# Performance work log

Hardware: AMD Instinct MI355X
Metric: run time of the kernel (lower is better)

## Reference

```python
import jax, jax.numpy as jnp
import numpy as np

B, D, H, W, C = 4, 8, 16, 16, 512
K_RED = 8
R = C // K_RED          # reduced channels for Q/K
EPS = 1e-3              # keras LayerNormalization default epsilon


def setup_inputs() -> dict:
    key = jax.random.key(0)
    ks = jax.random.split(key, 8)
    s = 0.02
    f32 = jnp.float32
    return {
        "x":  jax.random.normal(ks[0], (B, D, H, W, C), f32),
        # 1x1x1 Conv3D == per-position linear over channels
        "wq": (jax.random.normal(ks[1], (C, R), f32) * s), "bq": jnp.zeros((R,), f32),
        "wk": (jax.random.normal(ks[2], (C, R), f32) * s), "bk": jnp.zeros((R,), f32),
        "wv": (jax.random.normal(ks[3], (C, C), f32) * s), "bv": jnp.zeros((C,), f32),
        "wm": (jax.random.normal(ks[4], (C, C), f32) * s), "bm": jnp.zeros((C,), f32),
        "g1": jnp.ones((C,), f32), "b1": jnp.zeros((C,), f32),
        "g2": jnp.ones((C,), f32), "b2": jnp.zeros((C,), f32),
    }


def _layer_norm(x, g, b):
    m = jnp.mean(x, axis=-1, keepdims=True)
    v = jnp.mean(jnp.square(x - m), axis=-1, keepdims=True)
    return (x - m) * jax.lax.rsqrt(v + EPS) * g + b


def reference(x, wq, bq, wk, bk, wv, bv, wm, bm, g1, b1, g2, b2):
    b, d, h, w, c = x.shape
    f = h * w
    xf = x.reshape(b, d, f, c)                      # [B,D,F,C]
    Q = xf @ wq + bq                                # [B,D,F,R]
    K = xf @ wk + bk                                # [B,D,F,R]
    V = xf @ wv + bv                                # [B,D,F,C]
    # full global scores: [B, D, F, D, F]
    e = jnp.einsum('bifr,bgjr->bifgj', Q, K)
    alphas = jax.nn.softmax(e.reshape(b, d, f, d * f), axis=-1)
    alphas = alphas.reshape(b, d, f, d, f)
    # original einsum 'bdfgh,bdhi->bdfi' sums over key-depth g and uses V at
    # the query depth d; fold the g-sum first, then per-depth F x F matmul.
    a2 = alphas.sum(axis=3)                         # [B,D,F,F]
    attn = jnp.einsum('bdfh,bdhc->bdfc', a2, V)     # [B,D,F,C]
    y1 = _layer_norm(attn + xf, g1, b1)
    y2 = _layer_norm(y1 + jax.nn.relu(y1 @ wm + bm), g2, b2)
    return y2.reshape(b, d, h, w, c)
```

## Files before the change

kernel.cpp:

```cpp
#include <hip/hip_runtime.h>
#include <cstdint>

#define LN_EPS 1e-3f
using u16 = unsigned short;
using u32 = unsigned int;
typedef __attribute__((ext_vector_type(8))) short bh8;
typedef __attribute__((ext_vector_type(4))) float f4;
#define MFMA16(A,B,C) __builtin_amdgcn_mfma_f32_16x16x32_bf16((A),(B),(C),0,0,0)
#define LKBAR() do{ asm volatile("s_waitcnt lgkmcnt(0)" ::: "memory"); \
                    __builtin_amdgcn_s_barrier(); asm volatile("" ::: "memory"); }while(0)

__device__ __forceinline__ u16 bf16r(float f){
    union{float f;u32 u;} c; c.f=f;
    return (u16)((c.u + 0x7fffu + ((c.u>>16)&1u))>>16);
}
__device__ __forceinline__ u32 pk2(float a, float b){
    return (u32)bf16r(a) | ((u32)bf16r(b)<<16);
}

__global__ __launch_bounds__(256) void k0_prep(
    const float* __restrict__ wq, const float* __restrict__ wk,
    const float* __restrict__ wv, const float* __restrict__ wm,
    u16* __restrict__ wqkv_p, u16* __restrict__ wm_p)
{
    const int t = threadIdx.x;
    const int c = t & 15, qn = t >> 4;
    const int quad = qn & 3, ntl = qn >> 2;
    const int blk = blockIdx.x;
    if (blk < 32){
        const int s = blk >> 1, hh = blk & 1;
        const int krow = s*32 + quad*8;
        u16* dst = wqkv_p + (size_t)s*20480;
        #pragma unroll
        for (int i=0;i<5;++i){
            const int nt = hh*20 + i*4 + ntl;
            const int n = nt*16 + c;
            const float* src; int ldw;
            if (n < 64){ src = wq + (size_t)krow*64 + n; ldw = 64; }
            else if (n < 128){ src = wk + (size_t)krow*64 + (n-64); ldw = 64; }
            else { src = wv + (size_t)krow*512 + (n-128); ldw = 512; }
            float v[8];
            #pragma unroll
            for (int j=0;j<8;++j) v[j] = src[(size_t)j*ldw];
            uint4 o; o.x=pk2(v[0],v[1]); o.y=pk2(v[2],v[3]); o.z=pk2(v[4],v[5]); o.w=pk2(v[6],v[7]);
            *(uint4*)&dst[((nt*4+quad)*16 + c)*8] = o;
        }
    } else {
        const int bb = blk - 32;
        const int s = bb >> 1, hh = bb & 1;
        const int krow = s*32 + quad*8;
        u16* dst = wm_p + (size_t)s*16384;
        #pragma unroll
        for (int i=0;i<4;++i){
            const int nt = hh*16 + i*4 + ntl;
            const int n = nt*16 + c;
            const float* src = wm + (size_t)krow*512 + n;
            float v[8];
            #pragma unroll
            for (int j=0;j<8;++j) v[j] = src[(size_t)j*512];
            uint4 o; o.x=pk2(v[0],v[1]); o.y=pk2(v[2],v[3]); o.z=pk2(v[4],v[5]); o.w=pk2(v[6],v[7]);
            *(uint4*)&dst[((nt*4+quad)*16 + c)*8] = o;
        }
    }
}

__global__ __launch_bounds__(512) void k1_qkv(
    const float* __restrict__ x, const float* __restrict__ bq, const float* __restrict__ bk,
    const u16* __restrict__ wqkv_p,
    u16* __restrict__ Qb, u16* __restrict__ Kb, u16* __restrict__ Vb)
{
    __shared__ u16 Asf[16384];
    const int t = threadIdx.x, w = t>>6, lane = t&63, quad = (lane>>4)&3, c = lane&15;
    const int rowbase = blockIdx.x << 5;

    bh8 bw[5];
    #pragma unroll
    for (int nt2=0;nt2<5;++nt2)
        bw[nt2] = *(const bh8*)&wqkv_p[(size_t)((w*5+nt2)*4 + quad)*128 + c*8];
    #pragma unroll
    for (int i=0;i<8;++i){
        const int idx = t + (i<<9);
        const int fr = idx >> 7, fc4 = idx & 127;
        float4 xv = *(const float4*)&x[(size_t)(rowbase+fr)*512 + fc4*4];
        uint2 pkv; pkv.x = pk2(xv.x,xv.y); pkv.y = pk2(xv.z,xv.w);
        const int s = fc4 >> 3, qd = (fc4 >> 1) & 3, j0 = (fc4 & 1)*4;
        *(uint2*)&Asf[(fr>>4)*8192 + s*512 + (qd*16 + (fr&15))*8 + j0] = pkv;
    }
    f4 acc[2][5];
    #pragma unroll
    for (int rt=0;rt<2;++rt)
        #pragma unroll
        for (int i=0;i<5;++i) acc[rt][i] = (f4){0.f,0.f,0.f,0.f};
    __syncthreads();

    #pragma unroll
    for (int s=0;s<16;++s){
        bh8 bn[5];
        if (s+1 < 16){
            #pragma unroll
            for (int nt2=0;nt2<5;++nt2)
                bn[nt2] = *(const bh8*)&wqkv_p[(size_t)(s+1)*20480 + ((w*5+nt2)*4 + quad)*128 + c*8];
        }
        bh8 a[2];
        #pragma unroll
        for (int rt=0;rt<2;++rt)
            a[rt] = *(const bh8*)&Asf[rt*8192 + s*512 + (quad*16+c)*8];
        __builtin_amdgcn_s_setprio(1);
        #pragma unroll
        for (int rt=0;rt<2;++rt)
            #pragma unroll
            for (int nt2=0;nt2<5;++nt2)
                acc[rt][nt2] = MFMA16(a[rt], bw[nt2], acc[rt][nt2]);
        __builtin_amdgcn_s_setprio(0);
        if (s+1 < 16){
            #pragma unroll
            for (int nt2=0;nt2<5;++nt2) bw[nt2] = bn[nt2];
        }
    }

    const int bd = rowbase >> 8;
    #pragma unroll
    for (int rt=0;rt<2;++rt){
        const int rtg = (blockIdx.x<<1) + rt;
        const int kloc = (rowbase & 255) + rt*16 + quad*4;
        const int sv = kloc >> 5, kq = (kloc >> 3) & 3, jk0 = kloc & 7;
        #pragma unroll
        for (int nt2=0;nt2<5;++nt2){
            const int colb = w*80 + nt2*16;
            if (colb < 128){
                const bool isK = (colb >= 64);
                const int r = colb - (isK ? 64 : 0) + c;
                const float bias = isK ? bk[r] : bq[r];
                u16* dstb = (isK ? Kb : Qb) + ((size_t)(rtg*2 + (r>>5))*4 + ((r>>3)&3))*128 + (r&7);
                #pragma unroll
                for (int reg=0;reg<4;++reg)
                    dstb[(quad*4+reg)*8] = bf16r(acc[rt][nt2][reg] + bias);
            } else {
                const int ntv = (colb - 128) >> 4;
                u16* dstv = Vb + (size_t)bd*131072 + (size_t)sv*16384
                               + (size_t)((ntv*4+kq)*128 + c*8 + jk0);
                ushort4 o;
                o.x = bf16r(acc[rt][nt2][0]); o.y = bf16r(acc[rt][nt2][1]);
                o.z = bf16r(acc[rt][nt2][2]); o.w = bf16r(acc[rt][nt2][3]);
                *(ushort4*)dstv = o;
            }
        }
    }
}

__global__ __launch_bounds__(512) void k234(
    const u16* __restrict__ Qb, const u16* __restrict__ Kb, const u16* __restrict__ Vb,
    const u16* __restrict__ wm_p,
    const float* __restrict__ x, const float* __restrict__ bv,
    const float* __restrict__ g1, const float* __restrict__ b1,
    const float* __restrict__ bm, const float* __restrict__ g2, const float* __restrict__ b2,
    float* __restrict__ out)
{
    __shared__ u16 U[16384];
    __shared__ float redA[256], redB[256];
    const int t = threadIdx.x, w = t>>6, lane = t&63, quad = (lane>>4)&3, c = lane&15;
    const int bd = blockIdx.x & 31, ftile = blockIdx.x >> 5;
    const int b = bd >> 3;
    const int rowbase = (bd<<8) + (ftile<<5);
    const int rt00 = rowbase >> 4;
    const u16* Kp = Kb + (size_t)b*131072;
    const u16* Vp = Vb + (size_t)bd*131072;

    bh8 aq[2][2];
    #pragma unroll
    for (int rt=0;rt<2;++rt)
        #pragma unroll
        for (int kk=0;kk<2;++kk)
            aq[rt][kk] = *(const bh8*)&Qb[(size_t)(rt00+rt)*1024 + kk*512 + (quad*16+c)*8];

    float a2r[2][2][4] = {};
    bh8 bk0[2][2];
    #pragma unroll
    for (int kt=0;kt<2;++kt)
        #pragma unroll
        for (int kk=0;kk<2;++kk)
            bk0[kt][kk] = *(const bh8*)&Kp[(size_t)(w*2+kt)*1024 + kk*512 + (quad*16+c)*8];
    #pragma unroll
    for (int cc=0; cc<8; ++cc){
        bh8 bn[2][2];
        if (cc+1 < 8){
            #pragma unroll
            for (int kt=0;kt<2;++kt)
                #pragma unroll
                for (int kk=0;kk<2;++kk)
                    bn[kt][kk] = *(const bh8*)&Kp[(size_t)((cc+1)*16 + w*2+kt)*1024 + kk*512 + (quad*16+c)*8];
        }
        f4 sa[2][2];
        __builtin_amdgcn_s_setprio(1);
        #pragma unroll
        for (int rt=0;rt<2;++rt)
            #pragma unroll
            for (int kt=0;kt<2;++kt){
                sa[rt][kt] = (f4){0.f,0.f,0.f,0.f};
                sa[rt][kt] = MFMA16(aq[rt][0], bk0[kt][0], sa[rt][kt]);
                sa[rt][kt] = MFMA16(aq[rt][1], bk0[kt][1], sa[rt][kt]);
            }
        __builtin_amdgcn_s_setprio(0);
        #pragma unroll
        for (int rt=0;rt<2;++rt)
            #pragma unroll
            for (int kt=0;kt<2;++kt)
                #pragma unroll
                for (int reg=0;reg<4;++reg)
                    a2r[rt][kt][reg] += __expf(sa[rt][kt][reg]);
        if (cc+1 < 8){
            #pragma unroll
            for (int kt=0;kt<2;++kt)
                #pragma unroll
                for (int kk=0;kk<2;++kk) bk0[kt][kk] = bn[kt][kk];
        }
    }
    bh8 bv8[4];
    #pragma unroll
    for (int nt2=0;nt2<4;++nt2)
        bv8[nt2] = *(const bh8*)&Vp[(size_t)((w*4+nt2)*4 + quad)*128 + c*8];
    float lp[2][4];
    #pragma unroll
    for (int rt=0;rt<2;++rt)
        #pragma unroll
        for (int reg=0;reg<4;++reg){
            float v = a2r[rt][0][reg] + a2r[rt][1][reg];
            v += __shfl_xor(v,1,64); v += __shfl_xor(v,2,64);
            v += __shfl_xor(v,4,64); v += __shfl_xor(v,8,64);
            lp[rt][reg] = v;
        }
    if (c==0){
        #pragma unroll
        for (int rt=0;rt<2;++rt)
            #pragma unroll
            for (int reg=0;reg<4;++reg) redA[w*32 + rt*16 + quad*4+reg] = lp[rt][reg];
    }
    LKBAR();
    float fac[2][4];
    #pragma unroll
    for (int rt=0;rt<2;++rt)
        #pragma unroll
        for (int reg=0;reg<4;++reg){
            const int q = rt*16 + quad*4 + reg;
            float s = 0.f;
            #pragma unroll
            for (int ww=0;ww<8;++ww) s += redA[ww*32 + q];
            fac[rt][reg] = 1.f/s;
        }
    #pragma unroll
    for (int rt=0;rt<2;++rt)
        #pragma unroll
        for (int kt=0;kt<2;++kt)
            #pragma unroll
            for (int reg=0;reg<4;++reg){
                const int jp = w*32 + kt*16 + c;
                U[rt*4096 + (jp>>5)*512 + (((jp>>3)&3)*16 + quad*4+reg)*8 + (jp&7)]
                    = bf16r(a2r[rt][kt][reg]*fac[rt][reg]);
            }
    LKBAR();

    float xr[2][4][4];
    #pragma unroll
    for (int rt=0;rt<2;++rt)
        #pragma unroll
        for (int nt2=0;nt2<4;++nt2){
            const int col = w*64 + nt2*16 + c;
            #pragma unroll
            for (int reg=0;reg<4;++reg){
                const int row = rowbase + rt*16 + quad*4 + reg;
                xr[rt][nt2][reg] = x[(size_t)row*512 + col];
            }
        }

    f4 cacc[2][4];
    #pragma unroll
    for (int rt=0;rt<2;++rt)
        #pragma unroll
        for (int i=0;i<4;++i) cacc[rt][i] = (f4){0.f,0.f,0.f,0.f};
    #pragma unroll
    for (int s8=0;s8<8;++s8){
        bh8 bn[4];
        if (s8+1 < 8){
            #pragma unroll
            for (int nt2=0;nt2<4;++nt2)
                bn[nt2] = *(const bh8*)&Vp[(size_t)(s8+1)*16384 + ((w*4+nt2)*4 + quad)*128 + c*8];
        }
        bh8 a[2];
        #pragma unroll
        for (int rt=0;rt<2;++rt)
            a[rt] = *(const bh8*)&U[rt*4096 + s8*512 + (quad*16+c)*8];
        __builtin_amdgcn_s_setprio(1);
        #pragma unroll
        for (int rt=0;rt<2;++rt)
            #pragma unroll
            for (int nt2=0;nt2<4;++nt2)
                cacc[rt][nt2] = MFMA16(a[rt], bv8[nt2], cacc[rt][nt2]);
        __builtin_amdgcn_s_setprio(0);
        if (s8+1 < 8){
            #pragma unroll
            for (int nt2=0;nt2<4;++nt2) bv8[nt2] = bn[nt2];
        }
    }
    bh8 bm8[4];
    #pragma unroll
    for (int nt2=0;nt2<4;++nt2)
        bm8[nt2] = *(const bh8*)&wm_p[(size_t)((w*4+nt2)*4 + quad)*128 + c*8];

    float mean1[2][4], rstd1[2][4];
    {
        float sv4[2][4] = {}, qv2[2][4] = {};
        #pragma unroll
        for (int rt=0;rt<2;++rt)
            #pragma unroll
            for (int nt2=0;nt2<4;++nt2){
                const int col = w*64 + nt2*16 + c;
                const float bvv = bv[col];
                #pragma unroll
                for (int reg=0;reg<4;++reg){
                    float val = cacc[rt][nt2][reg] + bvv + xr[rt][nt2][reg];
                    cacc[rt][nt2][reg] = val;
                    sv4[rt][reg] += val; qv2[rt][reg] = fmaf(val,val,qv2[rt][reg]);
                }
            }
        #pragma unroll
        for (int rt=0;rt<2;++rt)
            #pragma unroll
            for (int reg=0;reg<4;++reg){
                float s1=sv4[rt][reg], s2=qv2[rt][reg];
                s1 += __shfl_xor(s1,1,64); s2 += __shfl_xor(s2,1,64);
                s1 += __shfl_xor(s1,2,64); s2 += __shfl_xor(s2,2,64);
                s1 += __shfl_xor(s1,4,64); s2 += __shfl_xor(s2,4,64);
                s1 += __shfl_xor(s1,8,64); s2 += __shfl_xor(s2,8,64);
                sv4[rt][reg]=s1; qv2[rt][reg]=s2;
            }
        if (c==0){
            #pragma unroll
            for (int rt=0;rt<2;++rt)
                #pragma unroll
                for (int reg=0;reg<4;++reg){
                    redA[w*32 + rt*16 + quad*4+reg]=sv4[rt][reg];
                    redB[w*32 + rt*16 + quad*4+reg]=qv2[rt][reg];
                }
        }
        LKBAR();
        #pragma unroll
        for (int rt=0;rt<2;++rt)
            #pragma unroll
            for (int reg=0;reg<4;++reg){
                const int q = rt*16 + quad*4 + reg;
                float S=0.f, Q2=0.f;
                #pragma unroll
                for (int ww=0;ww<8;++ww){ S += redA[ww*32+q]; Q2 += redB[ww*32+q]; }
                const float m = S*(1.f/512.f);
                mean1[rt][reg]=m; rstd1[rt][reg]=rsqrtf(Q2*(1.f/512.f) - m*m + LN_EPS);
            }
        #pragma unroll
        for (int rt=0;rt<2;++rt)
            #pragma unroll
            for (int nt2=0;nt2<4;++nt2){
                const int col = w*64 + nt2*16 + c;
                const float gg = g1[col], bb1 = b1[col];
                #pragma unroll
                for (int reg=0;reg<4;++reg){
                    float y = (cacc[rt][nt2][reg]-mean1[rt][reg])*rstd1[rt][reg]*gg + bb1;
                    cacc[rt][nt2][reg] = y;
                    U[rt*8192 + (col>>5)*512 + (((col>>3)&3)*16 + quad*4+reg)*8 + (col&7)] = bf16r(y);
                }
            }
        LKBAR();
    }

    f4 dacc[2][4];
    #pragma unroll
    for (int rt=0;rt<2;++rt)
        #pragma unroll
        for (int i=0;i<4;++i) dacc[rt][i] = (f4){0.f,0.f,0.f,0.f};
    #pragma unroll
    for (int s=0;s<16;++s){
        bh8 bn[4];
        if (s+1 < 16){
            #pragma unroll
            for (int nt2=0;nt2<4;++nt2)
                bn[nt2] = *(const bh8*)&wm_p[(size_t)(s+1)*16384 + ((w*4+nt2)*4 + quad)*128 + c*8];
        }
        bh8 a[2];
        #pragma unroll
        for (int rt=0;rt<2;++rt)
            a[rt] = *(const bh8*)&U[rt*8192 + s*512 + (quad*16+c)*8];
        __builtin_amdgcn_s_setprio(1);
        #pragma unroll
        for (int rt=0;rt<2;++rt)
            #pragma unroll
            for (int nt2=0;nt2<4;++nt2)
                dacc[rt][nt2] = MFMA16(a[rt], bm8[nt2], dacc[rt][nt2]);
        __builtin_amdgcn_s_setprio(0);
        if (s+1 < 16){
            #pragma unroll
            for (int nt2=0;nt2<4;++nt2) bm8[nt2] = bn[nt2];
        }
    }

    {
        float sv4[2][4] = {}, qv2[2][4] = {};
        #pragma unroll
        for (int rt=0;rt<2;++rt)
            #pragma unroll
            for (int nt2=0;nt2<4;++nt2){
                const int col = w*64 + nt2*16 + c;
                const float bmv = bm[col];
                #pragma unroll
                for (int reg=0;reg<4;++reg){
                    float hh = fmaxf(dacc[rt][nt2][reg]+bmv, 0.f) + cacc[rt][nt2][reg];
                    dacc[rt][nt2][reg] = hh;
                    sv4[rt][reg] += hh; qv2[rt][reg] = fmaf(hh,hh,qv2[rt][reg]);
                }
            }
        #pragma unroll
        for (int rt=0;rt<2;++rt)
            #pragma unroll
            for (int reg=0;reg<4;++reg){
                float s1=sv4[rt][reg], s2=qv2[rt][reg];
                s1 += __shfl_xor(s1,1,64); s2 += __shfl_xor(s2,1,64);
                s1 += __shfl_xor(s1,2,64); s2 += __shfl_xor(s2,2,64);
                s1 += __shfl_xor(s1,4,64); s2 += __shfl_xor(s2,4,64);
                s1 += __shfl_xor(s1,8,64); s2 += __shfl_xor(s2,8,64);
                sv4[rt][reg]=s1; qv2[rt][reg]=s2;
            }
        if (c==0){
            #pragma unroll
            for (int rt=0;rt<2;++rt)
                #pragma unroll
                for (int reg=0;reg<4;++reg){
                    redA[w*32 + rt*16 + quad*4+reg]=sv4[rt][reg];
                    redB[w*32 + rt*16 + quad*4+reg]=qv2[rt][reg];
                }
        }
        LKBAR();
        #pragma unroll
        for (int rt=0;rt<2;++rt){
            float mean[4], rstd[4];
            #pragma unroll
            for (int reg=0;reg<4;++reg){
                const int q = rt*16 + quad*4 + reg;
                float S=0.f, Q2=0.f;
                #pragma unroll
                for (int ww=0;ww<8;++ww){ S += redA[ww*32+q]; Q2 += redB[ww*32+q]; }
                const float m = S*(1.f/512.f);
                mean[reg]=m; rstd[reg]=rsqrtf(Q2*(1.f/512.f) - m*m + LN_EPS);
            }
            #pragma unroll
            for (int nt2=0;nt2<4;++nt2){
                const int col = w*64 + nt2*16 + c;
                const float gg = g2[col], bb2 = b2[col];
                #pragma unroll
                for (int reg=0;reg<4;++reg){
                    const int row = rowbase + rt*16 + quad*4 + reg;
                    out[(size_t)row*512 + col] = (dacc[rt][nt2][reg]-mean[reg])*rstd[reg]*gg + bb2;
                }
            }
        }
    }
}

extern "C" void kernel_launch(void* const* d_in, const int* in_sizes, int n_in,
                              void* d_out, int out_size, void* d_ws, size_t ws_size,
                              hipStream_t stream) {
    (void)in_sizes; (void)n_in; (void)out_size; (void)ws_size;
    const float* x  = (const float*)d_in[0];
    const float* wq = (const float*)d_in[1];
    const float* bq = (const float*)d_in[2];
    const float* wk = (const float*)d_in[3];
    const float* bk = (const float*)d_in[4];
    const float* wv = (const float*)d_in[5];
    const float* bv = (const float*)d_in[6];
    const float* wm = (const float*)d_in[7];
    const float* bm = (const float*)d_in[8];
    const float* g1 = (const float*)d_in[9];
    const float* b1 = (const float*)d_in[10];
    const float* g2 = (const float*)d_in[11];
    const float* b2 = (const float*)d_in[12];

    u16* wqkv_p = (u16*)d_ws;
    u16* wm_p   = wqkv_p + 327680;
    u16* Qb     = wm_p   + 262144;
    u16* Kb     = Qb     + 524288;
    u16* Vb     = Kb     + 524288;
    float* outp = (float*)d_out;

    k0_prep<<<64, 256, 0, stream>>>(wq, wk, wv, wm, wqkv_p, wm_p);
    k1_qkv <<<256, 512, 0, stream>>>(x, bq, bk, wqkv_p, Qb, Kb, Vb);
    k234   <<<256, 512, 0, stream>>>(Qb, Kb, Vb, wm_p, x, bv, g1, b1, bm, g2, b2, outp);
}
```

Before: 124.6 us.

## Fuse three kernels into one cooperative kernel with grid syncs

Merges the weight-prep, QKV projection and attention/LN/MLP kernels into a single cooperative launch of 256 blocks, separated by threadfence plus grid.sync barriers. The aim is to remove two kernel launch gaps and the inter-kernel drain/ramp. In exchange every block pays two grid-wide barriers. The fused kernel also needs both shared buffers at once, which raises LDS and register use per block and may cut occupancy.

```diff
diff --git a/kernel.cpp b/kernel.cpp
--- a/kernel.cpp
+++ b/kernel.cpp
@@ -1,6 +1,8 @@
 #include <hip/hip_runtime.h>
+#include <hip/hip_cooperative_groups.h>
 #include <cstdint>
 
+namespace cg = cooperative_groups;
 #define LN_EPS 1e-3f
 using u16 = unsigned short;
 using u32 = unsigned int;
@@ -18,444 +20,445 @@
     return (u32)bf16r(a) | ((u32)bf16r(b)<<16);
 }
 
-__global__ __launch_bounds__(256) void k0_prep(
-    const float* __restrict__ wq, const float* __restrict__ wk,
-    const float* __restrict__ wv, const float* __restrict__ wm,
-    u16* __restrict__ wqkv_p, u16* __restrict__ wm_p)
-{
-    const int t = threadIdx.x;
-    const int c = t & 15, qn = t >> 4;
-    const int quad = qn & 3, ntl = qn >> 2;
-    const int blk = blockIdx.x;
-    if (blk < 32){
-        const int s = blk >> 1, hh = blk & 1;
-        const int krow = s*32 + quad*8;
-        u16* dst = wqkv_p + (size_t)s*20480;
-        #pragma unroll
-        for (int i=0;i<5;++i){
-            const int nt = hh*20 + i*4 + ntl;
-            const int n = nt*16 + c;
-            const float* src; int ldw;
-            if (n < 64){ src = wq + (size_t)krow*64 + n; ldw = 64; }
-            else if (n < 128){ src = wk + (size_t)krow*64 + (n-64); ldw = 64; }
-            else { src = wv + (size_t)krow*512 + (n-128); ldw = 512; }
-            float v[8];
-            #pragma unroll
-            for (int j=0;j<8;++j) v[j] = src[(size_t)j*ldw];
-            uint4 o; o.x=pk2(v[0],v[1]); o.y=pk2(v[2],v[3]); o.z=pk2(v[4],v[5]); o.w=pk2(v[6],v[7]);
-            *(uint4*)&dst[((nt*4+quad)*16 + c)*8] = o;
-        }
-    } else {
-        const int bb = blk - 32;
-        const int s = bb >> 1, hh = bb & 1;
-        const int krow = s*32 + quad*8;
-        u16* dst = wm_p + (size_t)s*16384;
-        #pragma unroll
-        for (int i=0;i<4;++i){
-            const int nt = hh*16 + i*4 + ntl;
-            const int n = nt*16 + c;
-            const float* src = wm + (size_t)krow*512 + n;
-            float v[8];
-            #pragma unroll
-            for (int j=0;j<8;++j) v[j] = src[(size_t)j*512];
-            uint4 o; o.x=pk2(v[0],v[1]); o.y=pk2(v[2],v[3]); o.z=pk2(v[4],v[5]); o.w=pk2(v[6],v[7]);
-            *(uint4*)&dst[((nt*4+quad)*16 + c)*8] = o;
-        }
-    }
-}
-
-__global__ __launch_bounds__(512) void k1_qkv(
-    const float* __restrict__ x, const float* __restrict__ bq, const float* __restrict__ bk,
-    const u16* __restrict__ wqkv_p,
-    u16* __restrict__ Qb, u16* __restrict__ Kb, u16* __restrict__ Vb)
+__global__ __launch_bounds__(512) void fused_all(
+    const float* __restrict__ x,
+    const float* __restrict__ wq, const float* __restrict__ bq,
+    const float* __restrict__ wk, const float* __restrict__ bk,
+    const float* __restrict__ wv, const float* __restrict__ bv,
+    const float* __restrict__ wm, const float* __restrict__ bm,
+    const float* __restrict__ g1, const float* __restrict__ b1,
+    const float* __restrict__ g2, const float* __restrict__ b2,
+    u16* __restrict__ wqkv_p, u16* __restrict__ wm_p,
+    u16* __restrict__ Qb, u16* __restrict__ Kb, u16* __restrict__ Vb,
+    float* __restrict__ out)
 {
     __shared__ u16 Asf[16384];
-    const int t = threadIdx.x, w = t>>6, lane = t&63, quad = (lane>>4)&3, c = lane&15;
-    const int rowbase = blockIdx.x << 5;
-
-    bh8 bw[5];
-    #pragma unroll
-    for (int nt2=0;nt2<5;++nt2)
-        bw[nt2] = *(const bh8*)&wqkv_p[(size_t)((w*5+nt2)*4 + quad)*128 + c*8];
-    #pragma unroll
-    for (int i=0;i<8;++i){
-        const int idx = t + (i<<9);
-        const int fr = idx >> 7, fc4 = idx & 127;
-        float4 xv = *(const float4*)&x[(size_t)(rowbase+fr)*512 + fc4*4];
-        uint2 pkv; pkv.x = pk2(xv.x,xv.y); pkv.y = pk2(xv.z,xv.w);
-        const int s = fc4 >> 3, qd = (fc4 >> 1) & 3, j0 = (fc4 & 1)*4;
-        *(uint2*)&Asf[(fr>>4)*8192 + s*512 + (qd*16 + (fr&15))*8 + j0] = pkv;
-    }
-    f4 acc[2][5];
-    #pragma unroll
-    for (int rt=0;rt<2;++rt)
-        #pragma unroll
-        for (int i=0;i<5;++i) acc[rt][i] = (f4){0.f,0.f,0.f,0.f};
-    __syncthreads();
-
-    #pragma unroll
-    for (int s=0;s<16;++s){
-        bh8 bn[5];
-        if (s+1 < 16){
-            #pragma unroll
-            for (int nt2=0;nt2<5;++nt2)
-                bn[nt2] = *(const bh8*)&wqkv_p[(size_t)(s+1)*20480 + ((w*5+nt2)*4 + quad)*128 + c*8];
-        }
-        bh8 a[2];
-        #pragma unroll
-        for (int rt=0;rt<2;++rt)
-            a[rt] = *(const bh8*)&Asf[rt*8192 + s*512 + (quad*16+c)*8];
-        __builtin_amdgcn_s_setprio(1);
-        #pragma unroll
-        for (int rt=0;rt<2;++rt)
-            #pragma unroll
-            for (int nt2=0;nt2<5;++nt2)
-                acc[rt][nt2] = MFMA16(a[rt], bw[nt2], acc[rt][nt2]);
-        __builtin_amdgcn_s_setprio(0);
-        if (s+1 < 16){
-            #pragma unroll
-            for (int nt2=0;nt2<5;++nt2) bw[nt2] = bn[nt2];
-        }
-    }
-
-    const int bd = rowbase >> 8;
-    #pragma unroll
-    for (int rt=0;rt<2;++rt){
-        const int rtg = (blockIdx.x<<1) + rt;
-        const int kloc = (rowbase & 255) + rt*16 + quad*4;
-        const int sv = kloc >> 5, kq = (kloc >> 3) & 3, jk0 = kloc & 7;
-        #pragma unroll
-        for (int nt2=0;nt2<5;++nt2){
-            const int colb = w*80 + nt2*16;
-            if (colb < 128){
-                const bool isK = (colb >= 64);
-                const int r = colb - (isK ? 64 : 0) + c;
-                const float bias = isK ? bk[r] : bq[r];
-                u16* dstb = (isK ? Kb : Qb) + ((size_t)(rtg*2 + (r>>5))*4 + ((r>>3)&3))*128 + (r&7);
-                #pragma unroll
-                for (int reg=0;reg<4;++reg)
-                    dstb[(quad*4+reg)*8] = bf16r(acc[rt][nt2][reg] + bias);
-            } else {
-                const int ntv = (colb - 128) >> 4;
-                u16* dstv = Vb + (size_t)bd*131072 + (size_t)sv*16384
-                               + (size_t)((ntv*4+kq)*128 + c*8 + jk0);
-                ushort4 o;
-                o.x = bf16r(acc[rt][nt2][0]); o.y = bf16r(acc[rt][nt2][1]);
-                o.z = bf16r(acc[rt][nt2][2]); o.w = bf16r(acc[rt][nt2][3]);
-                *(ushort4*)dstv = o;
-            }
-        }
-    }
-}
-
-__global__ __launch_bounds__(512) void k234(
-    const u16* __restrict__ Qb, const u16* __restrict__ Kb, const u16* __restrict__ Vb,
-    const u16* __restrict__ wm_p,
-    const float* __restrict__ x, const float* __restrict__ bv,
-    const float* __restrict__ g1, const float* __restrict__ b1,
-    const float* __restrict__ bm, const float* __restrict__ g2, const float* __restrict__ b2,
-    float* __restrict__ out)
-{
     __shared__ u16 U[16384];
     __shared__ float redA[256], redB[256];
+    cg::grid_group grid = cg::this_grid();
     const int t = threadIdx.x, w = t>>6, lane = t&63, quad = (lane>>4)&3, c = lane&15;
-    const int bd = blockIdx.x & 31, ftile = blockIdx.x >> 5;
-    const int b = bd >> 3;
-    const int rowbase = (bd<<8) + (ftile<<5);
-    const int rt00 = rowbase >> 4;
-    const u16* Kp = Kb + (size_t)b*131072;
-    const u16* Vp = Vb + (size_t)bd*131072;
-
-    bh8 aq[2][2];
-    #pragma unroll
-    for (int rt=0;rt<2;++rt)
-        #pragma unroll
-        for (int kk=0;kk<2;++kk)
-            aq[rt][kk] = *(const bh8*)&Qb[(size_t)(rt00+rt)*1024 + kk*512 + (quad*16+c)*8];
-
-    float a2r[2][2][4] = {};
-    bh8 bk0[2][2];
-    #pragma unroll
-    for (int kt=0;kt<2;++kt)
-        #pragma unroll
-        for (int kk=0;kk<2;++kk)
-            bk0[kt][kk] = *(const bh8*)&Kp[(size_t)(w*2+kt)*1024 + kk*512 + (quad*16+c)*8];
-    #pragma unroll
-    for (int cc=0; cc<8; ++cc){
-        bh8 bn[2][2];
-        if (cc+1 < 8){
+
+    if (blockIdx.x < 64 && t < 256){
+        const int c0 = t & 15, qn = t >> 4;
+        const int q0 = qn & 3, ntl = qn >> 2;
+        const int blk = blockIdx.x;
+        if (blk < 32){
+            const int s = blk >> 1, hh = blk & 1;
+            const int krow = s*32 + q0*8;
+            u16* dst = wqkv_p + (size_t)s*20480;
+            #pragma unroll
+            for (int i=0;i<5;++i){
+                const int nt = hh*20 + i*4 + ntl;
+                const int n = nt*16 + c0;
+                const float* src; int ldw;
+                if (n < 64){ src = wq + (size_t)krow*64 + n; ldw = 64; }
+                else if (n < 128){ src = wk + (size_t)krow*64 + (n-64); ldw = 64; }
+                else { src = wv + (size_t)krow*512 + (n-128); ldw = 512; }
+                float v[8];
+                #pragma unroll
+                for (int j=0;j<8;++j) v[j] = src[(size_t)j*ldw];
+                uint4 o; o.x=pk2(v[0],v[1]); o.y=pk2(v[2],v[3]); o.z=pk2(v[4],v[5]); o.w=pk2(v[6],v[7]);
+                *(uint4*)&dst[((nt*4+q0)*16 + c0)*8] = o;
+            }
+        } else {
+            const int bb = blk - 32;
+            const int s = bb >> 1, hh = bb & 1;
+            const int krow = s*32 + q0*8;
+            u16* dst = wm_p + (size_t)s*16384;
+            #pragma unroll
+            for (int i=0;i<4;++i){
+                const int nt = hh*16 + i*4 + ntl;
+                const int n = nt*16 + c0;
+                const float* src = wm + (size_t)krow*512 + n;
+                float v[8];
+                #pragma unroll
+                for (int j=0;j<8;++j) v[j] = src[(size_t)j*512];
+                uint4 o; o.x=pk2(v[0],v[1]); o.y=pk2(v[2],v[3]); o.z=pk2(v[4],v[5]); o.w=pk2(v[6],v[7]);
+                *(uint4*)&dst[((nt*4+q0)*16 + c0)*8] = o;
+            }
+        }
+    }
+    __threadfence();
+    grid.sync();
+
+    {
+        const int rowbase = blockIdx.x << 5;
+        bh8 bw[5];
+        #pragma unroll
+        for (int nt2=0;nt2<5;++nt2)
+            bw[nt2] = *(const bh8*)&wqkv_p[(size_t)((w*5+nt2)*4 + quad)*128 + c*8];
+        #pragma unroll
+        for (int i=0;i<8;++i){
+            const int idx = t + (i<<9);
+            const int fr = idx >> 7, fc4 = idx & 127;
+            float4 xv = *(const float4*)&x[(size_t)(rowbase+fr)*512 + fc4*4];
+            uint2 pkv; pkv.x = pk2(xv.x,xv.y); pkv.y = pk2(xv.z,xv.w);
+            const int s = fc4 >> 3, qd = (fc4 >> 1) & 3, j0 = (fc4 & 1)*4;
+            *(uint2*)&Asf[(fr>>4)*8192 + s*512 + (qd*16 + (fr&15))*8 + j0] = pkv;
+        }
+        f4 acc[2][5];
+        #pragma unroll
+        for (int rt=0;rt<2;++rt)
+            #pragma unroll
+            for (int i=0;i<5;++i) acc[rt][i] = (f4){0.f,0.f,0.f,0.f};
+        __syncthreads();
+
+        #pragma unroll
+        for (int s=0;s<16;++s){
+            bh8 bn[5];
+            if (s+1 < 16){
+                #pragma unroll
+                for (int nt2=0;nt2<5;++nt2)
+                    bn[nt2] = *(const bh8*)&wqkv_p[(size_t)(s+1)*20480 + ((w*5+nt2)*4 + quad)*128 + c*8];
+            }
+            bh8 a[2];
+            #pragma unroll
+            for (int rt=0;rt<2;++rt)
+                a[rt] = *(const bh8*)&Asf[rt*8192 + s*512 + (quad*16+c)*8];
+            __builtin_amdgcn_s_setprio(1);
+            #pragma unroll
+            for (int rt=0;rt<2;++rt)
+                #pragma unroll
+                for (int nt2=0;nt2<5;++nt2)
+                    acc[rt][nt2] = MFMA16(a[rt], bw[nt2], acc[rt][nt2]);
+            __builtin_amdgcn_s_setprio(0);
+            if (s+1 < 16){
+                #pragma unroll
+                for (int nt2=0;nt2<5;++nt2) bw[nt2] = bn[nt2];
+            }
+        }
+
+        const int bd = rowbase >> 8;
+        #pragma unroll
+        for (int rt=0;rt<2;++rt){
+            const int rtg = (blockIdx.x<<1) + rt;
+            const int kloc = (rowbase & 255) + rt*16 + quad*4;
+            const int sv = kloc >> 5, kq = (kloc >> 3) & 3, jk0 = kloc & 7;
+            #pragma unroll
+            for (int nt2=0;nt2<5;++nt2){
+                const int colb = w*80 + nt2*16;
+                if (colb < 128){
+                    const bool isK = (colb >= 64);
+                    const int r = colb - (isK ? 64 : 0) + c;
+                    const float bias = isK ? bk[r] : bq[r];
+                    u16* dstb = (isK ? Kb : Qb) + ((size_t)(rtg*2 + (r>>5))*4 + ((r>>3)&3))*128 + (r&7);
+                    #pragma unroll
+                    for (int reg=0;reg<4;++reg)
+                        dstb[(quad*4+reg)*8] = bf16r(acc[rt][nt2][reg] + bias);
+                } else {
+                    const int ntv = (colb - 128) >> 4;
+                    u16* dstv = Vb + (size_t)bd*131072 + (size_t)sv*16384
+                                   + (size_t)((ntv*4+kq)*128 + c*8 + jk0);
+                    ushort4 o;
+                    o.x = bf16r(acc[rt][nt2][0]); o.y = bf16r(acc[rt][nt2][1]);
+                    o.z = bf16r(acc[rt][nt2][2]); o.w = bf16r(acc[rt][nt2][3]);
+                    *(ushort4*)dstv = o;
+                }
+            }
+        }
+    }
+    __threadfence();
+    grid.sync();
+
+    {
+        const int bd = blockIdx.x & 31, ftile = blockIdx.x >> 5;
+        const int b = bd >> 3;
+        const int rowbase = (bd<<8) + (ftile<<5);
+        const int rt00 = rowbase >> 4;
+        const u16* Kp = Kb + (size_t)b*131072;
+        const u16* Vp = Vb + (size_t)bd*131072;
+
+        bh8 aq[2][2];
+        #pragma unroll
+        for (int rt=0;rt<2;++rt)
+            #pragma unroll
+            for (int kk=0;kk<2;++kk)
+                aq[rt][kk] = *(const bh8*)&Qb[(size_t)(rt00+rt)*1024 + kk*512 + (quad*16+c)*8];
+
+        float a2r[2][2][4] = {};
+        bh8 bk0[2][2];
+        #pragma unroll
+        for (int kt=0;kt<2;++kt)
+            #pragma unroll
+            for (int kk=0;kk<2;++kk)
+                bk0[kt][kk] = *(const bh8*)&Kp[(size_t)(w*2+kt)*1024 + kk*512 + (quad*16+c)*8];
+        #pragma unroll
+        for (int cc=0; cc<8; ++cc){
+            bh8 bn[2][2];
+            if (cc+1 < 8){
+                #pragma unroll
+                for (int kt=0;kt<2;++kt)
+                    #pragma unroll
+                    for (int kk=0;kk<2;++kk)
+                        bn[kt][kk] = *(const bh8*)&Kp[(size_t)((cc+1)*16 + w*2+kt)*1024 + kk*512 + (quad*16+c)*8];
+            }
+            f4 sa[2][2];
+            __builtin_amdgcn_s_setprio(1);
+            #pragma unroll
+            for (int rt=0;rt<2;++rt)
+                #pragma unroll
+                for (int kt=0;kt<2;++kt){
+                    sa[rt][kt] = (f4){0.f,0.f,0.f,0.f};
+                    sa[rt][kt] = MFMA16(aq[rt][0], bk0[kt][0], sa[rt][kt]);
+                    sa[rt][kt] = MFMA16(aq[rt][1], bk0[kt][1], sa[rt][kt]);
+                }
+            __builtin_amdgcn_s_setprio(0);
+            #pragma unroll
+            for (int rt=0;rt<2;++rt)
+                #pragma unroll
+                for (int kt=0;kt<2;++kt)
+                    #pragma unroll
+                    for (int reg=0;reg<4;++reg)
+                        a2r[rt][kt][reg] += __expf(sa[rt][kt][reg]);
+            if (cc+1 < 8){
+                #pragma unroll
+                for (int kt=0;kt<2;++kt)
+                    #pragma unroll
+                    for (int kk=0;kk<2;++kk) bk0[kt][kk] = bn[kt][kk];
+            }
+        }
+        bh8 bv8[4];
+        #pragma unroll
+        for (int nt2=0;nt2<4;++nt2)
+            bv8[nt2] = *(const bh8*)&Vp[(size_t)((w*4+nt2)*4 + quad)*128 + c*8];
+        float lp[2][4];
+        #pragma unroll
+        for (int rt=0;rt<2;++rt)
+            #pragma unroll
+            for (int reg=0;reg<4;++reg){
+                float v = a2r[rt][0][reg] + a2r[rt][1][reg];
+                v += __shfl_xor(v,1,64); v += __shfl_xor(v,2,64);
+                v += __shfl_xor(v,4,64); v += __shfl_xor(v,8,64);
+                lp[rt][reg] = v;
+            }
+        if (c==0){
+            #pragma unroll
+            for (int rt=0;rt<2;++rt)
+                #pragma unroll
+                for (int reg=0;reg<4;++reg) redA[w*32 + rt*16 + quad*4+reg] = lp[rt][reg];
+        }
+        LKBAR();
+        float fac[2][4];
+        #pragma unroll
+        for (int rt=0;rt<2;++rt)
+            #pragma unroll
+            for (int reg=0;reg<4;++reg){
+                const int q = rt*16 + quad*4 + reg;
+                float s = 0.f;
+                #pragma unroll
+                for (int ww=0;ww<8;++ww) s += redA[ww*32 + q];
+                fac[rt][reg] = 1.f/s;
+            }
+        #pragma unroll
+        for (int rt=0;rt<2;++rt)
             #pragma unroll
             for (int kt=0;kt<2;++kt)
                 #pragma unroll
-                for (int kk=0;kk<2;++kk)
-                    bn[kt][kk] = *(const bh8*)&Kp[(size_t)((cc+1)*16 + w*2+kt)*1024 + kk*512 + (quad*16+c)*8];
-        }
-        f4 sa[2][2];
-        __builtin_amdgcn_s_setprio(1);
-        #pragma unroll
-        for (int rt=0;rt<2;++rt)
-            #pragma unroll
-            for (int kt=0;kt<2;++kt){
-                sa[rt][kt] = (f4){0.f,0.f,0.f,0.f};
-                sa[rt][kt] = MFMA16(aq[rt][0], bk0[kt][0], sa[rt][kt]);
-                sa[rt][kt] = MFMA16(aq[rt][1], bk0[kt][1], sa[rt][kt]);
-            }
-        __builtin_amdgcn_s_setprio(0);
-        #pragma unroll
-        for (int rt=0;rt<2;++rt)
-            #pragma unroll
-            for (int kt=0;kt<2;++kt)
-                #pragma unroll
-                for (int reg=0;reg<4;++reg)
-                    a2r[rt][kt][reg] += __expf(sa[rt][kt][reg]);
-        if (cc+1 < 8){
-            #pragma unroll
-            for (int kt=0;kt<2;++kt)
-                #pragma unroll
-                for (int kk=0;kk<2;++kk) bk0[kt][kk] = bn[kt][kk];
-        }
-    }
-    bh8 bv8[4];
-    #pragma unroll
-    for (int nt2=0;nt2<4;++nt2)
-        bv8[nt2] = *(const bh8*)&Vp[(size_t)((w*4+nt2)*4 + quad)*128 + c*8];
-    float lp[2][4];
-    #pragma unroll
-    for (int rt=0;rt<2;++rt)
-        #pragma unroll
-        for (int reg=0;reg<4;++reg){
-            float v = a2r[rt][0][reg] + a2r[rt][1][reg];
-            v += __shfl_xor(v,1,64); v += __shfl_xor(v,2,64);
-            v += __shfl_xor(v,4,64); v += __shfl_xor(v,8,64);
-            lp[rt][reg] = v;
-        }
-    if (c==0){
-        #pragma unroll
-        for (int rt=0;rt<2;++rt)
-            #pragma unroll
-            for (int reg=0;reg<4;++reg) redA[w*32 + rt*16 + quad*4+reg] = lp[rt][reg];
-    }
-    LKBAR();
-    float fac[2][4];
-    #pragma unroll
-    for (int rt=0;rt<2;++rt)
-        #pragma unroll
-        for (int reg=0;reg<4;++reg){
-            const int q = rt*16 + quad*4 + reg;
-            float s = 0.f;
-            #pragma unroll
-            for (int ww=0;ww<8;++ww) s += redA[ww*32 + q];
-            fac[rt][reg] = 1.f/s;
-        }
-    #pragma unroll
-    for (int rt=0;rt<2;++rt)
-        #pragma unroll
-        for (int kt=0;kt<2;++kt)
-            #pragma unroll
-            for (int reg=0;reg<4;++reg){
-                const int jp = w*32 + kt*16 + c;
-                U[rt*4096 + (jp>>5)*512 + (((jp>>3)&3)*16 + quad*4+reg)*8 + (jp&7)]
-                    = bf16r(a2r[rt][kt][reg]*fac[rt][reg]);
-            }
-    LKBAR();
-
-    float xr[2][4][4];
-    #pragma unroll
-    for (int rt=0;rt<2;++rt)
-        #pragma unroll
-        for (int nt2=0;nt2<4;++nt2){
-            const int col = w*64 + nt2*16 + c;
-            #pragma unroll
-            for (int reg=0;reg<4;++reg){
-                const int row = rowbase + rt*16 + quad*4 + reg;
-                xr[rt][nt2][reg] = x[(size_t)row*512 + col];
-            }
-        }
-
-    f4 cacc[2][4];
-    #pragma unroll
-    for (int rt=0;rt<2;++rt)
-        #pragma unroll
-        for (int i=0;i<4;++i) cacc[rt][i] = (f4){0.f,0.f,0.f,0.f};
-    #pragma unroll
-    for (int s8=0;s8<8;++s8){
-        bh8 bn[4];
-        if (s8+1 < 8){
-            #pragma unroll
-            for (int nt2=0;nt2<4;++nt2)
-                bn[nt2] = *(const bh8*)&Vp[(size_t)(s8+1)*16384 + ((w*4+nt2)*4 + quad)*128 + c*8];
-        }
-        bh8 a[2];
-        #pragma unroll
-        for (int rt=0;rt<2;++rt)
-            a[rt] = *(const bh8*)&U[rt*4096 + s8*512 + (quad*16+c)*8];
-        __builtin_amdgcn_s_setprio(1);
-        #pragma unroll
-        for (int rt=0;rt<2;++rt)
-            #pragma unroll
-            for (int nt2=0;nt2<4;++nt2)
-                cacc[rt][nt2] = MFMA16(a[rt], bv8[nt2], cacc[rt][nt2]);
-        __builtin_amdgcn_s_setprio(0);
-        if (s8+1 < 8){
-            #pragma unroll
-            for (int nt2=0;nt2<4;++nt2) bv8[nt2] = bn[nt2];
-        }
-    }
-    bh8 bm8[4];
-    #pragma unroll
-    for (int nt2=0;nt2<4;++nt2)
-        bm8[nt2] = *(const bh8*)&wm_p[(size_t)((w*4+nt2)*4 + quad)*128 + c*8];
-
-    float mean1[2][4], rstd1[2][4];
-    {
-        float sv4[2][4] = {}, qv2[2][4] = {};
+                for (int reg=0;reg<4;++reg){
+                    const int jp = w*32 + kt*16 + c;
+                    U[rt*4096 + (jp>>5)*512 + (((jp>>3)&3)*16 + quad*4+reg)*8 + (jp&7)]
+                        = bf16r(a2r[rt][kt][reg]*fac[rt][reg]);
+                }
+        LKBAR();
+
+        float xr[2][4][4];
         #pragma unroll
         for (int rt=0;rt<2;++rt)
             #pragma unroll
             for (int nt2=0;nt2<4;++nt2){
                 const int col = w*64 + nt2*16 + c;
-                const float bvv = bv[col];
-                #pragma unroll
-                for (int reg=0;reg<4;++reg){
-                    float val = cacc[rt][nt2][reg] + bvv + xr[rt][nt2][reg];
-                    cacc[rt][nt2][reg] = val;
-                    sv4[rt][reg] += val; qv2[rt][reg] = fmaf(val,val,qv2[rt][reg]);
-                }
-            }
-        #pragma unroll
-        for (int rt=0;rt<2;++rt)
-            #pragma unroll
-            for (int reg=0;reg<4;++reg){
-                float s1=sv4[rt][reg], s2=qv2[rt][reg];
-                s1 += __shfl_xor(s1,1,64); s2 += __shfl_xor(s2,1,64);
-                s1 += __shfl_xor(s1,2,64); s2 += __shfl_xor(s2,2,64);
-                s1 += __shfl_xor(s1,4,64); s2 += __shfl_xor(s2,4,64);
-                s1 += __shfl_xor(s1,8,64); s2 += __shfl_xor(s2,8,64);
-                sv4[rt][reg]=s1; qv2[rt][reg]=s2;
-            }
-        if (c==0){
-            #pragma unroll
-            for (int rt=0;rt<2;++rt)
-                #pragma unroll
-                for (int reg=0;reg<4;++reg){
-                    redA[w*32 + rt*16 + quad*4+reg]=sv4[rt][reg];
-                    redB[w*32 + rt*16 + quad*4+reg]=qv2[rt][reg];
-                }
-        }
-        LKBAR();
-        #pragma unroll
-        for (int rt=0;rt<2;++rt)
-            #pragma unroll
-            for (int reg=0;reg<4;++reg){
-                const int q = rt*16 + quad*4 + reg;
-                float S=0.f, Q2=0.f;
-                #pragma unroll
-                for (int ww=0;ww<8;++ww){ S += redA[ww*32+q]; Q2 += redB[ww*32+q]; }
-                const float m = S*(1.f/512.f);
-                mean1[rt][reg]=m; rstd1[rt][reg]=rsqrtf(Q2*(1.f/512.f) - m*m + LN_EPS);
-            }
-        #pragma unroll
-        for (int rt=0;rt<2;++rt)
-            #pragma unroll
-            for (int nt2=0;nt2<4;++nt2){
-                const int col = w*64 + nt2*16 + c;
-                const float gg = g1[col], bb1 = b1[col];
-                #pragma unroll
-                for (int reg=0;reg<4;++reg){
-                    float y = (cacc[rt][nt2][reg]-mean1[rt][reg])*rstd1[rt][reg]*gg + bb1;
-                    cacc[rt][nt2][reg] = y;
-                    U[rt*8192 + (col>>5)*512 + (((col>>3)&3)*16 + quad*4+reg)*8 + (col&7)] = bf16r(y);
-                }
-            }
-        LKBAR();
-    }
-
-    f4 dacc[2][4];
-    #pragma unroll
-    for (int rt=0;rt<2;++rt)
-        #pragma unroll
-        for (int i=0;i<4;++i) dacc[rt][i] = (f4){0.f,0.f,0.f,0.f};
-    #pragma unroll
-    for (int s=0;s<16;++s){
-        bh8 bn[4];
-        if (s+1 < 16){
-            #pragma unroll
-            for (int nt2=0;nt2<4;++nt2)
-                bn[nt2] = *(const bh8*)&wm_p[(size_t)(s+1)*16384 + ((w*4+nt2)*4 + quad)*128 + c*8];
-        }
-        bh8 a[2];
-        #pragma unroll
-        for (int rt=0;rt<2;++rt)
-            a[rt] = *(const bh8*)&U[rt*8192 + s*512 + (quad*16+c)*8];
-        __builtin_amdgcn_s_setprio(1);
-        #pragma unroll
-        for (int rt=0;rt<2;++rt)
-            #pragma unroll
-            for (int nt2=0;nt2<4;++nt2)
-                dacc[rt][nt2] = MFMA16(a[rt], bm8[nt2], dacc[rt][nt2]);
-        __builtin_amdgcn_s_setprio(0);
-        if (s+1 < 16){
-            #pragma unroll
-            for (int nt2=0;nt2<4;++nt2) bm8[nt2] = bn[nt2];
-        }
-    }
-
-    {
-        float sv4[2][4] = {}, qv2[2][4] = {};
-        #pragma unroll
-        for (int rt=0;rt<2;++rt)
-            #pragma unroll
-            for (int nt2=0;nt2<4;++nt2){
-                const int col = w*64 + nt2*16 + c;
-                const float bmv = bm[col];
-                #pragma unroll
-                for (int reg=0;reg<4;++reg){
-                    float hh = fmaxf(dacc[rt][nt2][reg]+bmv, 0.f) + cacc[rt][nt2][reg];
-                    dacc[rt][nt2][reg] = hh;
-                    sv4[rt][reg] += hh; qv2[rt][reg] = fmaf(hh,hh,qv2[rt][reg]);
-                }
-            }
-        #pragma unroll
-        for (int rt=0;rt<2;++rt)
-            #pragma unroll
-            for (int reg=0;reg<4;++reg){
-                float s1=sv4[rt][reg], s2=qv2[rt][reg];
-                s1 += __shfl_xor(s1,1,64); s2 += __shfl_xor(s2,1,64);
-                s1 += __shfl_xor(s1,2,64); s2 += __shfl_xor(s2,2,64);
-                s1 += __shfl_xor(s1,4,64); s2 += __shfl_xor(s2,4,64);
-                s1 += __shfl_xor(s1,8,64); s2 += __shfl_xor(s2,8,64);
-                sv4[rt][reg]=s1; qv2[rt][reg]=s2;
-            }
-        if (c==0){
-            #pragma unroll
-            for (int rt=0;rt<2;++rt)
-                #pragma unroll
-                for (int reg=0;reg<4;++reg){
-                    redA[w*32 + rt*16 + quad*4+reg]=sv4[rt][reg];
-                    redB[w*32 + rt*16 + quad*4+reg]=qv2[rt][reg];
-                }
-        }
-        LKBAR();
-        #pragma unroll
-        for (int rt=0;rt<2;++rt){
-            float mean[4], rstd[4];
-            #pragma unroll
-            for (int reg=0;reg<4;++reg){
-                const int q = rt*16 + quad*4 + reg;
-                float S=0.f, Q2=0.f;
-                #pragma unroll
-                for (int ww=0;ww<8;++ww){ S += redA[ww*32+q]; Q2 += redB[ww*32+q]; }
-                const float m = S*(1.f/512.f);
-                mean[reg]=m; rstd[reg]=rsqrtf(Q2*(1.f/512.f) - m*m + LN_EPS);
-            }
-            #pragma unroll
-            for (int nt2=0;nt2<4;++nt2){
-                const int col = w*64 + nt2*16 + c;
-                const float gg = g2[col], bb2 = b2[col];
                 #pragma unroll
                 for (int reg=0;reg<4;++reg){
                     const int row = rowbase + rt*16 + quad*4 + reg;
-                    out[(size_t)row*512 + col] = (dacc[rt][nt2][reg]-mean[reg])*rstd[reg]*gg + bb2;
+                    xr[rt][nt2][reg] = x[(size_t)row*512 + col];
+                }
+            }
+
+        f4 cacc[2][4];
+        #pragma unroll
+        for (int rt=0;rt<2;++rt)
+            #pragma unroll
+            for (int i=0;i<4;++i) cacc[rt][i] = (f4){0.f,0.f,0.f,0.f};
+        #pragma unroll
+        for (int s8=0;s8<8;++s8){
+            bh8 bn[4];
+            if (s8+1 < 8){
+                #pragma unroll
+                for (int nt2=0;nt2<4;++nt2)
+                    bn[nt2] = *(const bh8*)&Vp[(size_t)(s8+1)*16384 + ((w*4+nt2)*4 + quad)*128 + c*8];
+            }
+            bh8 a[2];
+            #pragma unroll
+            for (int rt=0;rt<2;++rt)
+                a[rt] = *(const bh8*)&U[rt*4096 + s8*512 + (quad*16+c)*8];
+            __builtin_amdgcn_s_setprio(1);
+            #pragma unroll
+            for (int rt=0;rt<2;++rt)
+                #pragma unroll
+                for (int nt2=0;nt2<4;++nt2)
+                    cacc[rt][nt2] = MFMA16(a[rt], bv8[nt2], cacc[rt][nt2]);
+            __builtin_amdgcn_s_setprio(0);
+            if (s8+1 < 8){
+                #pragma unroll
+                for (int nt2=0;nt2<4;++nt2) bv8[nt2] = bn[nt2];
+            }
+        }
+        bh8 bm8[4];
+        #pragma unroll
+        for (int nt2=0;nt2<4;++nt2)
+            bm8[nt2] = *(const bh8*)&wm_p[(size_t)((w*4+nt2)*4 + quad)*128 + c*8];
+
+        float mean1[2][4], rstd1[2][4];
+        {
+            float sv4[2][4] = {}, qv2[2][4] = {};
+            #pragma unroll
+            for (int rt=0;rt<2;++rt)
+                #pragma unroll
+                for (int nt2=0;nt2<4;++nt2){
+                    const int col = w*64 + nt2*16 + c;
+                    const float bvv = bv[col];
+                    #pragma unroll
+                    for (int reg=0;reg<4;++reg){
+                        float val = cacc[rt][nt2][reg] + bvv + xr[rt][nt2][reg];
+                        cacc[rt][nt2][reg] = val;
+                        sv4[rt][reg] += val; qv2[rt][reg] = fmaf(val,val,qv2[rt][reg]);
+                    }
+                }
+            #pragma unroll
+            for (int rt=0;rt<2;++rt)
+                #pragma unroll
+                for (int reg=0;reg<4;++reg){
+                    float s1=sv4[rt][reg], s2=qv2[rt][reg];
+                    s1 += __shfl_xor(s1,1,64); s2 += __shfl_xor(s2,1,64);
+                    s1 += __shfl_xor(s1,2,64); s2 += __shfl_xor(s2,2,64);
+                    s1 += __shfl_xor(s1,4,64); s2 += __shfl_xor(s2,4,64);
+                    s1 += __shfl_xor(s1,8,64); s2 += __shfl_xor(s2,8,64);
+                    sv4[rt][reg]=s1; qv2[rt][reg]=s2;
+                }
+            if (c==0){
+                #pragma unroll
+                for (int rt=0;rt<2;++rt)
+                    #pragma unroll
+                    for (int reg=0;reg<4;++reg){
+                        redA[w*32 + rt*16 + quad*4+reg]=sv4[rt][reg];
+                        redB[w*32 + rt*16 + quad*4+reg]=qv2[rt][reg];
+                    }
+            }
+            LKBAR();
+            #pragma unroll
+            for (int rt=0;rt<2;++rt)
+                #pragma unroll
+                for (int reg=0;reg<4;++reg){
+                    const int q = rt*16 + quad*4 + reg;
+                    float S=0.f, Q2=0.f;
+                    #pragma unroll
+                    for (int ww=0;ww<8;++ww){ S += redA[ww*32+q]; Q2 += redB[ww*32+q]; }
+                    const float m = S*(1.f/512.f);
+                    mean1[rt][reg]=m; rstd1[rt][reg]=rsqrtf(Q2*(1.f/512.f) - m*m + LN_EPS);
+                }
+            #pragma unroll
+            for (int rt=0;rt<2;++rt)
+                #pragma unroll
+                for (int nt2=0;nt2<4;++nt2){
+                    const int col = w*64 + nt2*16 + c;
+                    const float gg = g1[col], bb1 = b1[col];
+                    #pragma unroll
+                    for (int reg=0;reg<4;++reg){
+                        float y = (cacc[rt][nt2][reg]-mean1[rt][reg])*rstd1[rt][reg]*gg + bb1;
+                        cacc[rt][nt2][reg] = y;
+                        U[rt*8192 + (col>>5)*512 + (((col>>3)&3)*16 + quad*4+reg)*8 + (col&7)] = bf16r(y);
+                    }
+                }
+            LKBAR();
+        }
+
+        f4 dacc[2][4];
+        #pragma unroll
+        for (int rt=0;rt<2;++rt)
+            #pragma unroll
+            for (int i=0;i<4;++i) dacc[rt][i] = (f4){0.f,0.f,0.f,0.f};
+        #pragma unroll
+        for (int s=0;s<16;++s){
+            bh8 bn[4];
+            if (s+1 < 16){
+                #pragma unroll
+                for (int nt2=0;nt2<4;++nt2)
+                    bn[nt2] = *(const bh8*)&wm_p[(size_t)(s+1)*16384 + ((w*4+nt2)*4 + quad)*128 + c*8];
+            }
+            bh8 a[2];
+            #pragma unroll
+            for (int rt=0;rt<2;++rt)
+                a[rt] = *(const bh8*)&U[rt*8192 + s*512 + (quad*16+c)*8];
+            __builtin_amdgcn_s_setprio(1);
+            #pragma unroll
+            for (int rt=0;rt<2;++rt)
+                #pragma unroll
+                for (int nt2=0;nt2<4;++nt2)
+                    dacc[rt][nt2] = MFMA16(a[rt], bm8[nt2], dacc[rt][nt2]);
+            __builtin_amdgcn_s_setprio(0);
+            if (s+1 < 16){
+                #pragma unroll
+                for (int nt2=0;nt2<4;++nt2) bm8[nt2] = bn[nt2];
+            }
+        }
+
+        {
+            float sv4[2][4] = {}, qv2[2][4] = {};
+            #pragma unroll
+            for (int rt=0;rt<2;++rt)
+                #pragma unroll
+                for (int nt2=0;nt2<4;++nt2){
+                    const int col = w*64 + nt2*16 + c;
+                    const float bmv = bm[col];
+                    #pragma unroll
+                    for (int reg=0;reg<4;++reg){
+                        float hh = fmaxf(dacc[rt][nt2][reg]+bmv, 0.f) + cacc[rt][nt2][reg];
+                        dacc[rt][nt2][reg] = hh;
+                        sv4[rt][reg] += hh; qv2[rt][reg] = fmaf(hh,hh,qv2[rt][reg]);
+                    }
+                }
+            #pragma unroll
+            for (int rt=0;rt<2;++rt)
+                #pragma unroll
+                for (int reg=0;reg<4;++reg){
+                    float s1=sv4[rt][reg], s2=qv2[rt][reg];
+                    s1 += __shfl_xor(s1,1,64); s2 += __shfl_xor(s2,1,64);
+                    s1 += __shfl_xor(s1,2,64); s2 += __shfl_xor(s2,2,64);
+                    s1 += __shfl_xor(s1,4,64); s2 += __shfl_xor(s2,4,64);
+                    s1 += __shfl_xor(s1,8,64); s2 += __shfl_xor(s2,8,64);
+                    sv4[rt][reg]=s1; qv2[rt][reg]=s2;
+                }
+            if (c==0){
+                #pragma unroll
+                for (int rt=0;rt<2;++rt)
+                    #pragma unroll
+                    for (int reg=0;reg<4;++reg){
+                        redA[w*32 + rt*16 + quad*4+reg]=sv4[rt][reg];
+                        redB[w*32 + rt*16 + quad*4+reg]=qv2[rt][reg];
+                    }
+            }
+            LKBAR();
+            #pragma unroll
+            for (int rt=0;rt<2;++rt){
+                float mean[4], rstd[4];
+                #pragma unroll
+                for (int reg=0;reg<4;++reg){
+                    const int q = rt*16 + quad*4 + reg;
+                    float S=0.f, Q2=0.f;
+                    #pragma unroll
+                    for (int ww=0;ww<8;++ww){ S += redA[ww*32+q]; Q2 += redB[ww*32+q]; }
+                    const float m = S*(1.f/512.f);
+                    mean[reg]=m; rstd[reg]=rsqrtf(Q2*(1.f/512.f) - m*m + LN_EPS);
+                }
+                #pragma unroll
+                for (int nt2=0;nt2<4;++nt2){
+                    const int col = w*64 + nt2*16 + c;
+                    const float gg = g2[col], bb2 = b2[col];
+                    #pragma unroll
+                    for (int reg=0;reg<4;++reg){
+                        const int row = rowbase + rt*16 + quad*4 + reg;
+                        out[(size_t)row*512 + col] = (dacc[rt][nt2][reg]-mean[reg])*rstd[reg]*gg + bb2;
+                    }
                 }
             }
         }
@@ -487,7 +490,11 @@
     u16* Vb     = Kb     + 524288;
     float* outp = (float*)d_out;
 
-    k0_prep<<<64, 256, 0, stream>>>(wq, wk, wv, wm, wqkv_p, wm_p);
-    k1_qkv <<<256, 512, 0, stream>>>(x, bq, bk, wqkv_p, Qb, Kb, Vb);
-    k234   <<<256, 512, 0, stream>>>(Qb, Kb, Vb, wm_p, x, bv, g1, b1, bm, g2, b2, outp);
+    void* args[] = { (void*)&x, (void*)&wq, (void*)&bq, (void*)&wk, (void*)&bk,
+                     (void*)&wv, (void*)&bv, (void*)&wm, (void*)&bm,
+                     (void*)&g1, (void*)&b1, (void*)&g2, (void*)&b2,
+                     (void*)&wqkv_p, (void*)&wm_p,
+                     (void*)&Qb, (void*)&Kb, (void*)&Vb, (void*)&outp };
+    hipLaunchCooperativeKernel((const void*)fused_all, dim3(256), dim3(512),
+                               args, 0, stream);
 }
```

Result: slower. 316.4 us (+153.9%).
